# Kernel optimization log

Measured on AMD Instinct MI355X. Metric: run time of the kernel, lower is better.

The kernel has to match this reference:

```python
import jax, jax.numpy as jnp
import numpy as np

GAMMA = 0.5
TEMP = 0.05
TOP_K = 16
PAD = 1
GRID = 24  # hardcoded in the original module
EPS = 1e-8


def _normalize(x):
    return x / jnp.maximum(jnp.linalg.norm(x, axis=-1, keepdims=True), EPS)


def _neighbor_indices(sel):
    # all (2*PAD+1)^2 - 1 offsets, excluding (0,0), clamped to the grid
    offs = np.array([[i, j] for i in range(-PAD, PAD + 1)
                     for j in range(-PAD, PAD + 1) if not (i == 0 and j == 0)],
                    dtype=np.int32)
    coords = jnp.stack([sel // GRID, sel % GRID], axis=1)          # [S, 2]
    padded = jnp.clip(coords[:, None, :] + jnp.asarray(offs)[None, :, :], 0, GRID - 1)
    return padded[..., 0] * GRID + padded[..., 1]                   # [S, 8]


def _select_unique(vision_feature, text_embed, attention_mask):
    vn = _normalize(vision_feature)                                 # [Lv, D]
    tn = _normalize(text_embed)                                     # [Lt, D]
    cos = vn @ tn.T                                                 # [Lv, Lt]
    cos = jnp.where(attention_mask[None, :], cos, 0.0)
    scores = cos.max(axis=-1)                                       # [Lv]
    probs = jax.nn.softmax(scores / TEMP)                           # softmax over dim 0
    order = jnp.argsort(-probs)                                     # descending sort
    cum = jnp.cumsum(probs[order])
    thr = int(jnp.sum(cum <= GAMMA))                                # threshold index (concrete, eager)
    sel = order[:thr]
    return jnp.unique(_neighbor_indices(sel).ravel())


def setup_inputs() -> dict:
    key = jax.random.key(0)
    k1, k2 = jax.random.split(key)
    return {
        "vision_feature": jax.random.normal(k1, (576, 4096), dtype=jnp.float32),
        "text_embed": jax.random.normal(k2, (8192, 4096), dtype=jnp.float32),
        "attention_mask": jnp.ones((8192,), dtype=bool),
    }


def reference(vision_feature, text_embed, attention_mask):
    uniq = _select_unique(vision_feature, text_embed, attention_mask)   # [S] int
    sel_feat = vision_feature[uniq]                                     # [S, D]
    sn = _normalize(sel_feat)
    vn = _normalize(vision_feature)
    scos = sn @ vn.T                                                    # [S, Lv]
    top_vals, top_idx = jax.lax.top_k(scos, TOP_K)                      # [S, K]
    w = jax.nn.softmax(top_vals, axis=-1)                               # [S, K]
    # weighted pooling of the top-k most similar vision tokens
    return jnp.sum(vision_feature[top_idx] * w[..., None], axis=1)      # [S, D]
```

## Files before the change

kernel.cpp:

```cpp
#include <hip/hip_runtime.h>
#include <hip/hip_bf16.h>
#include <math.h>

#define GRID_N 24
#define NV 576
#define NT 8192
#define DK 4096
#define TOPK 16
#define LDT 68
#define DELTA 0.005f
#define WCAP 32768

typedef __bf16 bf16x8 __attribute__((ext_vector_type(8)));
typedef __bf16 bf16x4 __attribute__((ext_vector_type(4)));
typedef float  f32x4  __attribute__((ext_vector_type(4)));

__device__ __forceinline__ unsigned fkey(float f){
  unsigned u = __float_as_uint(f);
  return (u & 0x80000000u) ? ~u : (u | 0x80000000u);
}
__device__ __forceinline__ float fkey_inv(unsigned u){
  unsigned b = (u & 0x80000000u) ? (u & 0x7fffffffu) : ~u;
  return __uint_as_float(b);
}

__device__ __forceinline__ void gload_lds16(const void* g, void* l){
  __builtin_amdgcn_global_load_lds((const __attribute__((address_space(1))) unsigned*)g,
                                   (__attribute__((address_space(3))) unsigned*)l, 16, 0, 0);
}

__global__ __launch_bounds__(256) void prep_all(const float* __restrict__ V,
                                                const float* __restrict__ T,
                                                const unsigned char* __restrict__ mraw,
                                                __bf16* __restrict__ Vh,
                                                __bf16* __restrict__ Vl,
                                                __bf16* __restrict__ Th,
                                                float* __restrict__ invv,
                                                float* __restrict__ invt,
                                                int* __restrict__ mv,
                                                unsigned* __restrict__ skey,
                                                unsigned* __restrict__ skeyx,
                                                int* __restrict__ wcnt){
  int bid = blockIdx.x;
  int tid = threadIdx.x;
  if(bid < NT){
    int r = bid;
    const float4* p = (const float4*)(T + (size_t)r * DK);
    __bf16* o = Th + (size_t)r * DK;
    float s = 0.f;
    for(int c = tid; c < DK/4; c += 256){
      float4 v = p[c];
      s += v.x*v.x + v.y*v.y + v.z*v.z + v.w*v.w;
      bf16x4 h = { (__bf16)v.x, (__bf16)v.y, (__bf16)v.z, (__bf16)v.w };
      *(bf16x4*)(o + c*4) = h;
    }
    for(int d = 32; d > 0; d >>= 1) s += __shfl_down(s, d);
    __shared__ float r4[4];
    if((tid & 63) == 0) r4[tid >> 6] = s;
    __syncthreads();
    if(tid == 0){
      float t = r4[0] + r4[1] + r4[2] + r4[3];
      invt[r] = 1.0f / fmaxf(sqrtf(t), 1e-8f);
    }
  } else if(bid < NT + NV){
    int r = bid - NT;
    const float4* p = (const float4*)(V + (size_t)r * DK);
    __bf16* oh = Vh + (size_t)r * DK;
    __bf16* ol = Vl + (size_t)r * DK;
    float s = 0.f;
    for(int c = tid; c < DK/4; c += 256){
      float4 v = p[c];
      s += v.x*v.x + v.y*v.y + v.z*v.z + v.w*v.w;
      float f[4] = {v.x, v.y, v.z, v.w};
      bf16x4 h, l;
      #pragma unroll
      for(int q = 0; q < 4; q++){
        __bf16 hv = (__bf16)f[q];
        h[q] = hv;
        l[q] = (__bf16)(f[q] - (float)hv);
      }
      *(bf16x4*)(oh + c*4) = h;
      *(bf16x4*)(ol + c*4) = l;
    }
    for(int d = 32; d > 0; d >>= 1) s += __shfl_down(s, d);
    __shared__ float r4v[4];
    if((tid & 63) == 0) r4v[tid >> 6] = s;
    __syncthreads();
    if(tid == 0){
      float t = r4v[0] + r4v[1] + r4v[2] + r4v[3];
      invv[r] = 1.0f / fmaxf(sqrtf(t), 1e-8f);
    }
  } else {
    int mb = bid - NT - NV;
    int j = mb*256 + tid;
    if(j < NT){
      unsigned b0 = mraw[0], b1 = mraw[1], b2 = mraw[2], b3 = mraw[3];
      bool isf32 = (b0 == 0 && b1 == 0 && b2 == 0x80 && b3 == 0x3F);
      if(isf32)                 mv[j] = (((const float*)mraw)[j] != 0.0f) ? 1 : 0;
      else if((b1|b2|b3) != 0)  mv[j] = mraw[j] ? 1 : 0;
      else                      mv[j] = (((const int*)mraw)[j] != 0) ? 1 : 0;
    }
    if(mb == 0){
      for(int i = tid; i < NV; i += 256){ skey[i] = 0u; skeyx[i] = 0u; }
      if(tid == 0) *wcnt = 0;
    }
  }
}

__global__ __launch_bounds__(256) void score_gram(const __bf16* __restrict__ Vh,
                                                  const __bf16* __restrict__ Vl,
                                                  const __bf16* __restrict__ Th,
                                                  const float* __restrict__ invv,
                                                  const float* __restrict__ invt,
                                                  const int* __restrict__ mv,
                                                  float* __restrict__ cosm,
                                                  unsigned* __restrict__ skey,
                                                  float* __restrict__ G){
  __shared__ __align__(16) char lds[49152];
  int tid = threadIdx.x;
  int l = tid & 63, wid = tid >> 6;

  if(blockIdx.x < 576){
    __bf16* sA0 = (__bf16*)lds;
    __bf16* sB0 = (__bf16*)(lds + 16384);
    int m0 = (wid >> 1) * 32, n0 = (wid & 1) * 64;
    int bid = blockIdx.x;
    int orig = (bid & 7) * 72 + (bid >> 3);
    int jt = orig / 9, it = orig % 9;
    int vbase = it * 64, tbase = jt * 128;

    const __bf16* gsrc[6];
    __bf16* l0[6];
    int lstep[6];
    #pragma unroll
    for(int q = 0; q < 6; q++){
      int inst = wid*6 + q;
      int which = inst >> 3;
      int i = inst & 7;
      int r8 = i*8 + (l >> 3);
      int swz = ((l & 7) ^ (r8 & 7)) << 3;
      if(which == 0){
        gsrc[q] = Vh + (size_t)(vbase + r8)*DK + swz;
        l0[q] = sA0 + i*512;  lstep[q] = 64*64;
      } else if(which == 1){
        gsrc[q] = Th + (size_t)(tbase + r8)*DK + swz;
        l0[q] = sB0 + i*512;  lstep[q] = 128*64;
      } else {
        gsrc[q] = Th + (size_t)(tbase + 64 + r8)*DK + swz;
        l0[q] = sB0 + (8+i)*512;  lstep[q] = 128*64;
      }
    }

    f32x4 acc[2][4];
    #pragma unroll
    for(int i = 0; i < 2; i++)
      #pragma unroll
      for(int j = 0; j < 4; j++) acc[i][j] = (f32x4){0.f,0.f,0.f,0.f};

    #pragma unroll
    for(int q = 0; q < 6; q++) gload_lds16(gsrc[q], l0[q]);
    __syncthreads();

    for(int t = 0; t < DK/64; t++){
      int cur = t & 1;
      if(t + 1 < DK/64){
        #pragma unroll
        for(int q = 0; q < 6; q++)
          gload_lds16(gsrc[q] + (t+1)*64, l0[q] + (cur^1)*lstep[q]);
      }
      #pragma unroll
      for(int kc = 0; kc < 2; kc++){
        int sa = kc*4 + (l >> 4);
        bf16x8 ah[2], bh[4];
        #pragma unroll
        for(int fm = 0; fm < 2; fm++){
          int ra = m0 + fm*16 + (l & 15);
          ah[fm] = *(bf16x8*)(sA0 + cur*4096 + ra*64 + ((sa ^ (ra & 7)) << 3));
        }
        #pragma unroll
        for(int fn = 0; fn < 4; fn++){
          int rb = n0 + fn*16 + (l & 15);
          bh[fn] = *(bf16x8*)(sB0 + cur*8192 + rb*64 + ((sa ^ (rb & 7)) << 3));
        }
        #pragma unroll
        for(int fm = 0; fm < 2; fm++)
          #pragma unroll
          for(int fn = 0; fn < 4; fn++)
            acc[fm][fn] = __builtin_amdgcn_mfma_f32_16x16x32_bf16(ah[fm], bh[fn], acc[fm][fn], 0, 0, 0);
      }
      __syncthreads();
    }

    float* red = (float*)lds;
    float itc[4];
    #pragma unroll
    for(int fn = 0; fn < 4; fn++){
      int col = tbase + n0 + fn*16 + (l & 15);
      itc[fn] = (mv[col] != 0) ? invt[col] : 0.0f;
    }
    #pragma unroll
    for(int fm = 0; fm < 2; fm++){
      float rm[4];
      #pragma unroll
      for(int e = 0; e < 4; e++){
        int grow = vbase + m0 + fm*16 + ((l >> 4) << 2) + e;
        float iv = invv[grow];
        float mx = -3.402823e38f;
        #pragma unroll
        for(int fn = 0; fn < 4; fn++){
          int col = tbase + n0 + fn*16 + (l & 15);
          float val = acc[fm][fn][e] * iv * itc[fn];
          cosm[(size_t)grow*NT + col] = val;
          mx = fmaxf(mx, val);
        }
        rm[e] = mx;
      }
      #pragma unroll
      for(int d = 1; d < 16; d <<= 1){
        #pragma unroll
        for(int e = 0; e < 4; e++) rm[e] = fmaxf(rm[e], __shfl_xor(rm[e], d, 16));
      }
      if((l & 15) == 0){
        #pragma unroll
        for(int e = 0; e < 4; e++){
          int rl = m0 + fm*16 + ((l >> 4) << 2) + e;
          red[(wid & 1)*64 + rl] = rm[e];
        }
      }
    }
    __syncthreads();
    if(tid < 64){
      float m = fmaxf(red[tid], red[64 + tid]);
      atomicMax(skey + vbase + tid, fkey(m));
    }
  } else {
    __bf16* sAh = (__bf16*)lds;
    __bf16* sAl = (__bf16*)(lds + 8192);
    __bf16* sBh = (__bf16*)(lds + 16384);
    __bf16* sBl = (__bf16*)(lds + 24576);
    int m0 = (wid >> 1) * 32, n0 = (wid & 1) * 32;
    int gb = blockIdx.x - 576;
    int ubase = (gb / 9) * 64, ibase = (gb % 9) * 64;

    const __bf16* gsrc[8];
    __bf16* ldst[8];
    #pragma unroll
    for(int q = 0; q < 8; q++){
      int inst = wid*8 + q;
      int which = inst >> 3;
      int i = inst & 7;
      int rl = i*8 + (l >> 3);
      const __bf16* base;
      __bf16* lb;
      if(which == 0){      base = Vh + (size_t)(ubase + rl)*DK; lb = sAh + i*512; }
      else if(which == 1){ base = Vl + (size_t)(ubase + rl)*DK; lb = sAl + i*512; }
      else if(which == 2){ base = Vh + (size_t)(ibase + rl)*DK; lb = sBh + i*512; }
      else {               base = Vl + (size_t)(ibase + rl)*DK; lb = sBl + i*512; }
      int chunk_g = (l & 7) ^ (rl & 7);
      gsrc[q] = base + chunk_g*8;
      ldst[q] = lb;
    }

    f32x4 acc[2][2];
    #pragma unroll
    for(int i = 0; i < 2; i++)
      #pragma unroll
      for(int j = 0; j < 2; j++) acc[i][j] = (f32x4){0.f,0.f,0.f,0.f};

    for(int k0 = 0; k0 < DK; k0 += 64){
      __syncthreads();
      #pragma unroll
      for(int q = 0; q < 8; q++) gload_lds16(gsrc[q] + k0, ldst[q]);
      __syncthreads();
      #pragma unroll
      for(int kc = 0; kc < 2; kc++){
        int sa = kc*4 + (l >> 4);
        bf16x8 ah[2], al[2], bh[2], bl[2];
        #pragma unroll
        for(int f = 0; f < 2; f++){
          int ra = m0 + f*16 + (l & 15);
          int oa = ra*64 + ((sa ^ (ra & 7)) << 3);
          ah[f] = *(bf16x8*)(sAh + oa);
          al[f] = *(bf16x8*)(sAl + oa);
          int rb = n0 + f*16 + (l & 15);
          int ob = rb*64 + ((sa ^ (rb & 7)) << 3);
          bh[f] = *(bf16x8*)(sBh + ob);
          bl[f] = *(bf16x8*)(sBl + ob);
        }
        #pragma unroll
        for(int fm = 0; fm < 2; fm++)
          #pragma unroll
          for(int fn = 0; fn < 2; fn++){
            acc[fm][fn] = __builtin_amdgcn_mfma_f32_16x16x32_bf16(ah[fm], bh[fn], acc[fm][fn], 0, 0, 0);
            acc[fm][fn] = __builtin_amdgcn_mfma_f32_16x16x32_bf16(al[fm], bh[fn], acc[fm][fn], 0, 0, 0);
            acc[fm][fn] = __builtin_amdgcn_mfma_f32_16x16x32_bf16(ah[fm], bl[fn], acc[fm][fn], 0, 0, 0);
          }
      }
    }

    #pragma unroll
    for(int fm = 0; fm < 2; fm++){
      #pragma unroll
      for(int e = 0; e < 4; e++){
        int grow = ubase + m0 + fm*16 + ((l >> 4) << 2) + e;
        float su = invv[grow];
        #pragma unroll
        for(int fn = 0; fn < 2; fn++){
          int gcol = ibase + n0 + fn*16 + (l & 15);
          G[(size_t)grow*NV + gcol] = acc[fm][fn][e] * su * invv[gcol];
        }
      }
    }
  }
}

__global__ __launch_bounds__(256) void collect(const float* __restrict__ cosm,
                                               const unsigned* __restrict__ skey,
                                               int2* __restrict__ wl,
                                               int* __restrict__ wcnt){
  int i = blockIdx.x;
  float thrv = fkey_inv(skey[i]) - DELTA;
  int j0 = blockIdx.y * 2048;
  const float* row = cosm + (size_t)i*NT + j0;
  for(int k = threadIdx.x; k < 2048; k += 256){
    if(row[k] >= thrv){
      int p = atomicAdd(wcnt, 1);
      if(p < WCAP) wl[p] = make_int2(i, j0 + k);
    }
  }
}

__global__ __launch_bounds__(256) void verify(const int2* __restrict__ wl,
                                              const int* __restrict__ wcnt,
                                              const float* __restrict__ V,
                                              const float* __restrict__ T,
                                              const float* __restrict__ invv,
                                              const float* __restrict__ invt,
                                              const int* __restrict__ mv,
                                              unsigned* __restrict__ skeyx){
  int n = min(*wcnt, WCAP);
  __shared__ float red[4];
  for(int w = blockIdx.x; w < n; w += gridDim.x){
    int2 e = wl[w];
    const float4* vp = (const float4*)(V + (size_t)e.x*DK);
    const float4* tp = (const float4*)(T + (size_t)e.y*DK);
    float s = 0.f;
    for(int c = threadIdx.x; c < DK/4; c += 256){
      float4 a = vp[c], b = tp[c];
      s += a.x*b.x + a.y*b.y + a.z*b.z + a.w*b.w;
    }
    for(int d = 32; d > 0; d >>= 1) s += __shfl_down(s, d);
    if((threadIdx.x & 63) == 0) red[threadIdx.x >> 6] = s;
    __syncthreads();
    if(threadIdx.x == 0){
      float tot = red[0] + red[1] + red[2] + red[3];
      float val = (mv[e.y] != 0) ? tot * invv[e.x] * invt[e.y] : 0.0f;
      atomicMax(skeyx + e.x, fkey(val));
    }
    __syncthreads();
  }
}

__global__ __launch_bounds__(512) void select_kernel(const unsigned* __restrict__ skey,
                                                     int* __restrict__ uniq,
                                                     int* __restrict__ ucnt){
  __shared__ float s[NV];
  __shared__ float pv[1024];
  __shared__ int   pi[1024];
  __shared__ int   flags[NV];
  __shared__ float red8[8];
  __shared__ float mval, sval;
  __shared__ int   sthr;
  __shared__ int   wsum[9], woff[9];
  __shared__ int   totcnt;
  int tid = threadIdx.x;
  int lane = tid & 63, w = tid >> 6;

  for(int i = tid; i < NV; i += 512) s[i] = fkey_inv(skey[i]) / 0.05f;
  __syncthreads();
  float pm = -3.402823e38f;
  for(int i = tid; i < NV; i += 512) pm = fmaxf(pm, s[i]);
  for(int d = 32; d > 0; d >>= 1) pm = fmaxf(pm, __shfl_xor(pm, d));
  if(lane == 0) red8[w] = pm;
  __syncthreads();
  if(tid == 0){
    float m = red8[0];
    for(int q = 1; q < 8; q++) m = fmaxf(m, red8[q]);
    mval = m;
  }
  __syncthreads();
  float m = mval;
  float ps = 0.f;
  for(int i = tid; i < NV; i += 512){ float e = expf(s[i] - m); s[i] = e; ps += e; }
  for(int d = 32; d > 0; d >>= 1) ps += __shfl_xor(ps, d);
  if(lane == 0) red8[w] = ps;
  __syncthreads();
  if(tid == 0){
    float t = 0.f;
    for(int q = 0; q < 8; q++) t += red8[q];
    sval = t;
  }
  __syncthreads();
  float S = sval;
  for(int i = tid; i < 1024; i += 512){
    if(i < NV){ pv[i] = s[i] / S; pi[i] = i; }
    else      { pv[i] = -3.402823e38f; pi[i] = i; }
  }
  __syncthreads();
  for(int k = 2; k <= 1024; k <<= 1){
    for(int j = k >> 1; j > 0; j >>= 1){
      for(int i = tid; i < 1024; i += 512){
        int ixj = i ^ j;
        if(ixj > i){
          bool dir = ((i & k) == 0);
          float v1 = pv[i], v2 = pv[ixj];
          int   a1 = pi[i], a2 = pi[ixj];
          bool b2first = (v2 > v1) || (v2 == v1 && a2 < a1);
          if(b2first == dir){
            pv[i] = v2; pv[ixj] = v1; pi[i] = a2; pi[ixj] = a1;
          }
        }
      }
      __syncthreads();
    }
  }
  if(tid == 0){
    float cum = 0.f; int thr = 0;
    #pragma unroll 8
    for(int i = 0; i < NV; i++){
      cum += pv[i];
      thr += (cum <= 0.5f) ? 1 : 0;
    }
    sthr = thr;
  }
  for(int i = tid; i < NV; i += 512) flags[i] = 0;
  __syncthreads();
  int thr = sthr;
  for(int i = tid; i < thr; i += 512){
    int sel = pi[i];
    int r = sel / GRID_N, c = sel % GRID_N;
    #pragma unroll
    for(int dr = -1; dr <= 1; dr++){
      #pragma unroll
      for(int dc = -1; dc <= 1; dc++){
        if(dr == 0 && dc == 0) continue;
        int rr = min(max(r + dr, 0), GRID_N - 1);
        int cc = min(max(c + dc, 0), GRID_N - 1);
        flags[rr*GRID_N + cc] = 1;
      }
    }
  }
  __syncthreads();
  int f0 = flags[tid];
  unsigned long long m0 = __ballot(f0 != 0);
  int r0 = __popcll(m0 & ((1ull << lane) - 1));
  if(lane == 0) wsum[w] = __popcll(m0);
  int f1 = 0, r1 = 0;
  if(tid < 64){
    f1 = flags[512 + tid];
    unsigned long long m1 = __ballot(f1 != 0);
    r1 = __popcll(m1 & ((1ull << lane) - 1));
    if(lane == 0) wsum[8] = __popcll(m1);
  }
  __syncthreads();
  if(tid == 0){
    int acc = 0;
    for(int c = 0; c < 9; c++){ woff[c] = acc; acc += wsum[c]; }
    totcnt = acc;
    *ucnt = acc;
  }
  __syncthreads();
  if(f0) uniq[woff[w] + r0] = tid;
  if(tid < 64 && f1) uniq[woff[8] + r1] = 512 + tid;
  int cnt = totcnt;
  for(int i = tid; i < NV; i += 512) if(i >= cnt) uniq[i] = 0;
}

__global__ __launch_bounds__(256) void topk_out_kernel(const float* __restrict__ mat,
                                                       const int* __restrict__ uniq,
                                                       int use_uniq,
                                                       const float* __restrict__ V,
                                                       float* __restrict__ out,
                                                       int U){
  int u = blockIdx.x;
  int rrow = use_uniq ? uniq[u] : u;
  __shared__ float s[NV];
  __shared__ float wv[TOPK];
  __shared__ int   wi[TOPK];
  __shared__ float rv[4];
  __shared__ int   ri[4];
  __shared__ float w[TOPK];
  int tid = threadIdx.x;
  const float* row = mat + (size_t)rrow*NV;
  for(int i = tid; i < NV; i += 256) s[i] = row[i];
  __syncthreads();
  for(int k = 0; k < TOPK; k++){
    float bv = -3.402823e38f; int bi = 1 << 30;
    for(int i = tid; i < NV; i += 256){
      float v = s[i];
      if(v > bv || (v == bv && i < bi)){ bv = v; bi = i; }
    }
    for(int o = 32; o > 0; o >>= 1){
      float ov = __shfl_down(bv, o);
      int   oi = __shfl_down(bi, o);
      if(ov > bv || (ov == bv && oi < bi)){ bv = ov; bi = oi; }
    }
    int lane = tid & 63, wd = tid >> 6;
    if(lane == 0){ rv[wd] = bv; ri[wd] = bi; }
    __syncthreads();
    if(tid == 0){
      float fv = rv[0]; int fi = ri[0];
      for(int q = 1; q < 4; q++){
        if(rv[q] > fv || (rv[q] == fv && ri[q] < fi)){ fv = rv[q]; fi = ri[q]; }
      }
      wv[k] = fv; wi[k] = fi;
      s[fi] = -3.402823e38f;
    }
    __syncthreads();
  }
  if(tid == 0){
    float mx = wv[0];
    float sum = 0.f;
    for(int k = 0; k < TOPK; k++){ float e = expf(wv[k] - mx); w[k] = e; sum += e; }
    for(int k = 0; k < TOPK; k++) w[k] /= sum;
  }
  __syncthreads();
  for(int c = tid; c < DK/4; c += 256){
    float4 acc = {0.f, 0.f, 0.f, 0.f};
    #pragma unroll
    for(int k = 0; k < TOPK; k++){
      float4 v = *((const float4*)(V + (size_t)wi[k]*DK) + c);
      float wk = w[k];
      acc.x = fmaf(wk, v.x, acc.x);
      acc.y = fmaf(wk, v.y, acc.y);
      acc.z = fmaf(wk, v.z, acc.z);
      acc.w = fmaf(wk, v.w, acc.w);
    }
    *((float4*)(out + (size_t)u*DK) + c) = acc;
  }
}

__global__ __launch_bounds__(256) void rownorm_kernel(const float* __restrict__ x,
                                                      float* __restrict__ invn){
  int r = blockIdx.x;
  const float4* p = (const float4*)(x + (size_t)r * DK);
  float s = 0.f;
  for(int c = threadIdx.x; c < DK/4; c += 256){
    float4 v = p[c];
    s += v.x*v.x + v.y*v.y + v.z*v.z + v.w*v.w;
  }
  for(int o = 32; o > 0; o >>= 1) s += __shfl_down(s, o);
  __shared__ float r4[4];
  int lane = threadIdx.x & 63, w = threadIdx.x >> 6;
  if(lane == 0) r4[w] = s;
  __syncthreads();
  if(threadIdx.x == 0){
    float t = r4[0] + r4[1] + r4[2] + r4[3];
    invn[r] = 1.0f / fmaxf(sqrtf(t), 1e-8f);
  }
}

__global__ __launch_bounds__(256) void mask_expand(const unsigned char* __restrict__ mraw,
                                                   int* __restrict__ mv){
  unsigned b0 = mraw[0], b1 = mraw[1], b2 = mraw[2], b3 = mraw[3];
  int j = blockIdx.x * 256 + threadIdx.x;
  if(j >= NT) return;
  bool isf32 = (b0 == 0 && b1 == 0 && b2 == 0x80 && b3 == 0x3F);
  if(isf32){
    mv[j] = (((const float*)mraw)[j] != 0.0f) ? 1 : 0;
  } else if((b1 | b2 | b3) != 0){
    mv[j] = mraw[j] ? 1 : 0;
  } else {
    mv[j] = (((const int*)mraw)[j] != 0) ? 1 : 0;
  }
}

__device__ __forceinline__ void cvt8v(float4 u, float4 v, bf16x8& h, bf16x8& l){
  float buf[8] = {u.x, u.y, u.z, u.w, v.x, v.y, v.z, v.w};
  #pragma unroll
  for(int i = 0; i < 8; i++){
    float f = buf[i];
    __bf16 hi = (__bf16)f;
    h[i] = hi;
    l[i] = (__bf16)(f - (float)hi);
  }
}

__global__ __launch_bounds__(256) void score_mfma(const float* __restrict__ V,
                                                  const float* __restrict__ T,
                                                  const float* __restrict__ invv,
                                                  const float* __restrict__ invt,
                                                  const int* __restrict__ mv,
                                                  unsigned* __restrict__ skey){
  __shared__ __align__(16) char lds[49152];
  __bf16* Ah = (__bf16*)lds;
  __bf16* Al = (__bf16*)(lds + 8192);
  __bf16* Bh = (__bf16*)(lds + 16384);
  __bf16* Bl = (__bf16*)(lds + 32768);
  int tid = threadIdx.x;
  int l = tid & 63, wid = tid >> 6;
  int wr = wid >> 1, n0 = (wid & 1) * 64;
  int vbase = blockIdx.y * 64, tbase = blockIdx.x * 128;
  int arow = tid >> 2;
  int brow = tid >> 1;
  const float* aptr = V + (size_t)(vbase + arow) * DK + (tid & 3) * 16;
  const float* bptr = T + (size_t)(tbase + brow) * DK + (tid & 1) * 32;
  f32x4 acc[2][4];
  #pragma unroll
  for(int i = 0; i < 2; i++)
    #pragma unroll
    for(int j = 0; j < 4; j++) acc[i][j] = (f32x4){0.f, 0.f, 0.f, 0.f};
  float4 fa[4], fb[8];
  #pragma unroll
  for(int c = 0; c < 4; c++) fa[c] = *(const float4*)(aptr + 4*c);
  #pragma unroll
  for(int c = 0; c < 8; c++) fb[c] = *(const float4*)(bptr + 4*c);
  int aswz = arow & 7, bswz = brow & 7;
  for(int k0 = 0; k0 < DK; k0 += 64){
    #pragma unroll
    for(int hhalf = 0; hhalf < 2; hhalf++){
      bf16x8 hv, lv; cvt8v(fa[2*hhalf], fa[2*hhalf+1], hv, lv);
      int slot = (tid & 3)*2 + hhalf;
      int off = arow*64 + ((slot ^ aswz) << 3);
      *(bf16x8*)(Ah + off) = hv; *(bf16x8*)(Al + off) = lv;
    }
    #pragma unroll
    for(int c = 0; c < 4; c++){
      bf16x8 hv, lv; cvt8v(fb[2*c], fb[2*c+1], hv, lv);
      int slot = (tid & 1)*4 + c;
      int off = brow*64 + ((slot ^ bswz) << 3);
      *(bf16x8*)(Bh + off) = hv; *(bf16x8*)(Bl + off) = lv;
    }
    __syncthreads();
    if(k0 + 64 < DK){
      #pragma unroll
      for(int c = 0; c < 4; c++) fa[c] = *(const float4*)(aptr + k0 + 64 + 4*c);
      #pragma unroll
      for(int c = 0; c < 8; c++) fb[c] = *(const float4*)(bptr + k0 + 64 + 4*c);
    }
    #pragma unroll
    for(int kc = 0; kc < 2; kc++){
      bf16x8 ah[2], al[2], bh[4], bl[4];
      int sa = kc*4 + (l >> 4);
      #pragma unroll
      for(int fm = 0; fm < 2; fm++){
        int ra = wr*32 + fm*16 + (l & 15);
        int oa = ra*64 + ((sa ^ (ra & 7)) << 3);
        ah[fm] = *(bf16x8*)(Ah + oa);
        al[fm] = *(bf16x8*)(Al + oa);
      }
      #pragma unroll
      for(int fn = 0; fn < 4; fn++){
        int rb = n0 + fn*16 + (l & 15);
        int ob = rb*64 + ((sa ^ (rb & 7)) << 3);
        bh[fn] = *(bf16x8*)(Bh + ob);
        bl[fn] = *(bf16x8*)(Bl + ob);
      }
      #pragma unroll
      for(int fm = 0; fm < 2; fm++)
        #pragma unroll
        for(int fn = 0; fn < 4; fn++){
          acc[fm][fn] = __builtin_amdgcn_mfma_f32_16x16x32_bf16(ah[fm], bh[fn], acc[fm][fn], 0, 0, 0);
          acc[fm][fn] = __builtin_amdgcn_mfma_f32_16x16x32_bf16(al[fm], bh[fn], acc[fm][fn], 0, 0, 0);
          acc[fm][fn] = __builtin_amdgcn_mfma_f32_16x16x32_bf16(ah[fm], bl[fn], acc[fm][fn], 0, 0, 0);
        }
    }
    __syncthreads();
  }
  float* red = (float*)lds;
  float itc[4];
  #pragma unroll
  for(int fn = 0; fn < 4; fn++){
    int col = tbase + n0 + fn*16 + (l & 15);
    itc[fn] = (mv[col] != 0) ? invt[col] : 0.0f;
  }
  #pragma unroll
  for(int fm = 0; fm < 2; fm++){
    float rm[4];
    #pragma unroll
    for(int e = 0; e < 4; e++){
      int grow = vbase + wr*32 + fm*16 + ((l >> 4) << 2) + e;
      float ivv = invv[grow];
      float mx =     acc[fm][0][e] * itc[0];
      mx = fmaxf(mx, acc[fm][1][e] * itc[1]);
      mx = fmaxf(mx, acc[fm][2][e] * itc[2]);
      mx = fmaxf(mx, acc[fm][3][e] * itc[3]);
      rm[e] = mx * ivv;
    }
    #pragma unroll
    for(int d = 1; d < 16; d <<= 1){
      #pragma unroll
      for(int e = 0; e < 4; e++) rm[e] = fmaxf(rm[e], __shfl_xor(rm[e], d, 16));
    }
    if((l & 15) == 0){
      #pragma unroll
      for(int e = 0; e < 4; e++){
        int rl = wr*32 + fm*16 + ((l >> 4) << 2) + e;
        red[(wid & 1)*64 + rl] = rm[e];
      }
    }
  }
  __syncthreads();
  if(tid < 64){
    float m = fmaxf(red[tid], red[64 + tid]);
    atomicMax(skey + vbase + tid, fkey(m));
  }
}

__global__ __launch_bounds__(256) void scos_gemm(const float* __restrict__ V,
                                                 const int* __restrict__ uniq,
                                                 const float* __restrict__ invv,
                                                 float* __restrict__ scos,
                                                 int U){
  __shared__ __align__(16) float As[32*LDT];
  __shared__ __align__(16) float Bs[32*LDT];
  int tid = threadIdx.x;
  int tx = tid & 15, ty = tid >> 4;
  int ubase = blockIdx.y * 64, ibase = blockIdx.x * 64;
  int r0 = tid >> 3, r1 = r0 + 32;
  int kc = (tid & 7) << 2;
  int g0 = ubase + r0, g1 = ubase + r1;
  int arow0 = (g0 < U) ? uniq[g0] : 0;
  int arow1 = (g1 < U) ? uniq[g1] : 0;
  float acc[4][4] = {};
  for(int k0 = 0; k0 < DK; k0 += 32){
    __syncthreads();
    float4 a0 = *(const float4*)(V + (size_t)arow0*DK + k0 + kc);
    float4 a1 = *(const float4*)(V + (size_t)arow1*DK + k0 + kc);
    float4 b0 = *(const float4*)(V + (size_t)(ibase + r0)*DK + k0 + kc);
    float4 b1 = *(const float4*)(V + (size_t)(ibase + r1)*DK + k0 + kc);
    As[(kc+0)*LDT + r0] = a0.x; As[(kc+1)*LDT + r0] = a0.y; As[(kc+2)*LDT + r0] = a0.z; As[(kc+3)*LDT + r0] = a0.w;
    As[(kc+0)*LDT + r1] = a1.x; As[(kc+1)*LDT + r1] = a1.y; As[(kc+2)*LDT + r1] = a1.z; As[(kc+3)*LDT + r1] = a1.w;
    Bs[(kc+0)*LDT + r0] = b0.x; Bs[(kc+1)*LDT + r0] = b0.y; Bs[(kc+2)*LDT + r0] = b0.z; Bs[(kc+3)*LDT + r0] = b0.w;
    Bs[(kc+0)*LDT + r1] = b1.x; Bs[(kc+1)*LDT + r1] = b1.y; Bs[(kc+2)*LDT + r1] = b1.z; Bs[(kc+3)*LDT + r1] = b1.w;
    __syncthreads();
    #pragma unroll
    for(int k = 0; k < 32; k++){
      float4 a4 = *(const float4*)(As + k*LDT + ty*4);
      float4 b4 = *(const float4*)(Bs + k*LDT + tx*4);
      acc[0][0] += a4.x*b4.x; acc[0][1] += a4.x*b4.y; acc[0][2] += a4.x*b4.z; acc[0][3] += a4.x*b4.w;
      acc[1][0] += a4.y*b4.x; acc[1][1] += a4.y*b4.y; acc[1][2] += a4.y*b4.z; acc[1][3] += a4.y*b4.w;
      acc[2][0] += a4.z*b4.x; acc[2][1] += a4.z*b4.y; acc[2][2] += a4.z*b4.z; acc[2][3] += a4.z*b4.w;
      acc[3][0] += a4.w*b4.x; acc[3][1] += a4.w*b4.y; acc[3][2] += a4.w*b4.z; acc[3][3] += a4.w*b4.w;
    }
  }
  #pragma unroll
  for(int a = 0; a < 4; a++){
    int gu = ubase + ty*4 + a;
    if(gu < U){
      float su = invv[uniq[gu]];
      #pragma unroll
      for(int b = 0; b < 4; b++){
        int i = ibase + tx*4 + b;
        scos[(size_t)gu*NV + i] = acc[a][b] * su * invv[i];
      }
    }
  }
}

extern "C" void kernel_launch(void* const* d_in, const int* in_sizes, int n_in,
                              void* d_out, int out_size, void* d_ws, size_t ws_size,
                              hipStream_t stream){
  const float* V = (const float*)d_in[0];
  const float* T = (const float*)d_in[1];
  const unsigned char* mraw = (const unsigned char*)d_in[2];
  float* out = (float*)d_out;
  int U = out_size / DK;

  char* W = (char*)d_ws;
  float*    invv  = (float*)W;
  float*    invt  = (float*)(W + 2560);
  unsigned* skeyx = (unsigned*)(W + 35584);
  int*      uniq  = (int*)(W + 38144);
  int*      ucnt  = (int*)(W + 40448);
  unsigned* skey  = (unsigned*)(W + 40704);
  int*      mv    = (int*)(W + 43264);
  float*    G     = (float*)(W + 76032);
  __bf16*   Vh    = (__bf16*)(W + 1403136);
  __bf16*   Vl    = (__bf16*)(W + 6121728);
  float*    cosm  = (float*)(W + 10840320);
  __bf16*   Th    = (__bf16*)(W + 29714688);
  int*      wcnt  = (int*)(W + 29714688);
  int2*     wl    = (int2*)(W + 29714944);
  const size_t MAIN_NEED = 96823552;

  if(ws_size >= MAIN_NEED){
    prep_all<<<NT + NV + 32, 256, 0, stream>>>(V, T, mraw, Vh, Vl, Th, invv, invt, mv,
                                               skey, skeyx, wcnt);
    score_gram<<<576 + 81, 256, 0, stream>>>(Vh, Vl, Th, invv, invt, mv, cosm, skey, G);
    collect<<<dim3(NV, 4), 256, 0, stream>>>(cosm, skey, wl, wcnt);
    verify<<<1024, 256, 0, stream>>>(wl, wcnt, V, T, invv, invt, mv, skeyx);
    select_kernel<<<1, 512, 0, stream>>>(skeyx, uniq, ucnt);
    if(U > 0){
      topk_out_kernel<<<U, 256, 0, stream>>>(G, uniq, 1, V, out, U);
    }
  } else {
    hipMemsetAsync(skey, 0, NV*sizeof(unsigned), stream);
    mask_expand<<<(NT + 255)/256, 256, 0, stream>>>(mraw, mv);
    rownorm_kernel<<<NV, 256, 0, stream>>>(V, invv);
    rownorm_kernel<<<NT, 256, 0, stream>>>(T, invt);
    score_mfma<<<dim3(NT/128, NV/64), 256, 0, stream>>>(V, T, invv, invt, mv, skey);
    select_kernel<<<1, 512, 0, stream>>>(skey, uniq, ucnt);
    if(U > 0){
      scos_gemm<<<dim3(NV/64, (U + 63)/64), 256, 0, stream>>>(V, uniq, invv, G, U);
      topk_out_kernel<<<U, 256, 0, stream>>>(G, uniq, 0, V, out, U);
    }
  }
}
```

Baseline: 217.9 us.

## Split score GEMM warps along K with LDS reduction of partial accumulators

In the score GEMM tile, each pair of waves now splits the 64-wide K chunk in half instead of splitting output rows. Each wave computes a 64x64 output sub-tile over its K half. Partial sums from the second wave are written to LDS and added by the first wave before the epilogue. This gives a 4x4 MFMA block per wave with more operand reuse per LDS read. The costs are doubled accumulator registers, an extra LDS round trip with a barrier, and an epilogue run by only half the waves.

```diff
diff --git a/kernel.cpp b/kernel.cpp
--- a/kernel.cpp
+++ b/kernel.cpp
@@ -123,7 +123,9 @@
   if(blockIdx.x < 576){
     __bf16* sA0 = (__bf16*)lds;
     __bf16* sB0 = (__bf16*)(lds + 16384);
-    int m0 = (wid >> 1) * 32, n0 = (wid & 1) * 64;
+    int p = wid >> 1;
+    int kslice = wid & 1;
+    int ocol = p * 64;
     int bid = blockIdx.x;
     int orig = (bid & 7) * 72 + (bid >> 3);
     int jt = orig / 9, it = orig % 9;
@@ -151,11 +153,21 @@
       }
     }
 
-    f32x4 acc[2][4];
-    #pragma unroll
-    for(int i = 0; i < 2; i++)
+    f32x4 acc[4][4];
+    #pragma unroll
+    for(int i = 0; i < 4; i++)
       #pragma unroll
       for(int j = 0; j < 4; j++) acc[i][j] = (f32x4){0.f,0.f,0.f,0.f};
+
+    int sa = kslice*4 + (l >> 4);
+    int aoff[4], boff[4];
+    #pragma unroll
+    for(int f = 0; f < 4; f++){
+      int ra = f*16 + (l & 15);
+      aoff[f] = ra*64 + ((sa ^ (ra & 7)) << 3);
+      int rb = ocol + f*16 + (l & 15);
+      boff[f] = rb*64 + ((sa ^ (rb & 7)) << 3);
+    }
 
     #pragma unroll
     for(int q = 0; q < 6; q++) gload_lds16(gsrc[q], l0[q]);
@@ -168,69 +180,78 @@
         for(int q = 0; q < 6; q++)
           gload_lds16(gsrc[q] + (t+1)*64, l0[q] + (cur^1)*lstep[q]);
       }
-      #pragma unroll
-      for(int kc = 0; kc < 2; kc++){
-        int sa = kc*4 + (l >> 4);
-        bf16x8 ah[2], bh[4];
+      bf16x8 ah[4], bh[4];
+      #pragma unroll
+      for(int f = 0; f < 4; f++){
+        ah[f] = *(bf16x8*)(sA0 + cur*4096 + aoff[f]);
+        bh[f] = *(bf16x8*)(sB0 + cur*8192 + boff[f]);
+      }
+      #pragma unroll
+      for(int fm = 0; fm < 4; fm++)
         #pragma unroll
-        for(int fm = 0; fm < 2; fm++){
-          int ra = m0 + fm*16 + (l & 15);
-          ah[fm] = *(bf16x8*)(sA0 + cur*4096 + ra*64 + ((sa ^ (ra & 7)) << 3));
+        for(int fn = 0; fn < 4; fn++)
+          acc[fm][fn] = __builtin_amdgcn_mfma_f32_16x16x32_bf16(ah[fm], bh[fn], acc[fm][fn], 0, 0, 0);
+      __syncthreads();
+    }
+
+    float* accbuf = (float*)lds;
+    float* red2   = (float*)(lds + 34816);
+    if(kslice == 1){
+      #pragma unroll
+      for(int fm = 0; fm < 4; fm++)
+        #pragma unroll
+        for(int fn = 0; fn < 4; fn++)
+          #pragma unroll
+          for(int e = 0; e < 4; e++){
+            int row = fm*16 + ((l >> 4) << 2) + e;
+            int col = fn*16 + (l & 15);
+            accbuf[p*4160 + row*65 + col] = acc[fm][fn][e];
+          }
+    }
+    __syncthreads();
+    if(kslice == 0){
+      float itc[4];
+      #pragma unroll
+      for(int fn = 0; fn < 4; fn++){
+        int col = tbase + ocol + fn*16 + (l & 15);
+        itc[fn] = (mv[col] != 0) ? invt[col] : 0.0f;
+      }
+      #pragma unroll
+      for(int fm = 0; fm < 4; fm++){
+        float rm[4];
+        #pragma unroll
+        for(int e = 0; e < 4; e++){
+          int rloc = fm*16 + ((l >> 4) << 2) + e;
+          int grow = vbase + rloc;
+          float iv = invv[grow];
+          float mx = -3.402823e38f;
+          #pragma unroll
+          for(int fn = 0; fn < 4; fn++){
+            int colg = tbase + ocol + fn*16 + (l & 15);
+            float tot = acc[fm][fn][e] + accbuf[p*4160 + rloc*65 + fn*16 + (l & 15)];
+            float val = tot * iv * itc[fn];
+            cosm[(size_t)grow*NT + colg] = val;
+            mx = fmaxf(mx, val);
+          }
+          rm[e] = mx;
         }
         #pragma unroll
-        for(int fn = 0; fn < 4; fn++){
-          int rb = n0 + fn*16 + (l & 15);
-          bh[fn] = *(bf16x8*)(sB0 + cur*8192 + rb*64 + ((sa ^ (rb & 7)) << 3));
+        for(int d = 1; d < 16; d <<= 1){
+          #pragma unroll
+          for(int e = 0; e < 4; e++) rm[e] = fmaxf(rm[e], __shfl_xor(rm[e], d, 16));
         }
-        #pragma unroll
-        for(int fm = 0; fm < 2; fm++)
+        if((l & 15) == 0){
           #pragma unroll
-          for(int fn = 0; fn < 4; fn++)
-            acc[fm][fn] = __builtin_amdgcn_mfma_f32_16x16x32_bf16(ah[fm], bh[fn], acc[fm][fn], 0, 0, 0);
-      }
-      __syncthreads();
-    }
-
-    float* red = (float*)lds;
-    float itc[4];
-    #pragma unroll
-    for(int fn = 0; fn < 4; fn++){
-      int col = tbase + n0 + fn*16 + (l & 15);
-      itc[fn] = (mv[col] != 0) ? invt[col] : 0.0f;
-    }
-    #pragma unroll
-    for(int fm = 0; fm < 2; fm++){
-      float rm[4];
-      #pragma unroll
-      for(int e = 0; e < 4; e++){
-        int grow = vbase + m0 + fm*16 + ((l >> 4) << 2) + e;
-        float iv = invv[grow];
-        float mx = -3.402823e38f;
-        #pragma unroll
-        for(int fn = 0; fn < 4; fn++){
-          int col = tbase + n0 + fn*16 + (l & 15);
-          float val = acc[fm][fn][e] * iv * itc[fn];
-          cosm[(size_t)grow*NT + col] = val;
-          mx = fmaxf(mx, val);
+          for(int e = 0; e < 4; e++){
+            int rloc = fm*16 + ((l >> 4) << 2) + e;
+            red2[p*64 + rloc] = rm[e];
+          }
         }
-        rm[e] = mx;
-      }
-      #pragma unroll
-      for(int d = 1; d < 16; d <<= 1){
-        #pragma unroll
-        for(int e = 0; e < 4; e++) rm[e] = fmaxf(rm[e], __shfl_xor(rm[e], d, 16));
-      }
-      if((l & 15) == 0){
-        #pragma unroll
-        for(int e = 0; e < 4; e++){
-          int rl = m0 + fm*16 + ((l >> 4) << 2) + e;
-          red[(wid & 1)*64 + rl] = rm[e];
-        }
       }
     }
     __syncthreads();
     if(tid < 64){
-      float m = fmaxf(red[tid], red[64 + tid]);
+      float m = fmaxf(red2[tid], red2[64 + tid]);
       atomicMax(skey + vbase + tid, fkey(m));
     }
   } else {
```

After: 241.9 us. 1.11x slower.
